# Optimization experiments

Measured on AMD Instinct MI355X. Metric: run time of the kernel, lower is better.

Reference implementation:

```python
import jax, jax.numpy as jnp
import numpy as np

D = 1024
H = 16
HD = D // H
FF = 2 * D
EPS = 1e-5


def _ln(x, g, b):
    mu = jnp.mean(x, axis=-1, keepdims=True)
    var = jnp.mean(jnp.square(x - mu), axis=-1, keepdims=True)
    return (x - mu) * jax.lax.rsqrt(var + EPS) * g + b


def setup_inputs() -> dict:
    key = jax.random.key(0)
    ks = jax.random.split(key, 16)
    s = 1.0 / np.sqrt(D)
    sf = 1.0 / np.sqrt(FF)
    inp = {
        "x": jax.random.normal(ks[0], (4, 2048, D), dtype=jnp.float32),
        "Wq": jax.random.uniform(ks[1], (D, D), jnp.float32, -s, s),
        "bq": jnp.zeros((D,), jnp.float32),
        "Wk": jax.random.uniform(ks[2], (D, D), jnp.float32, -s, s),
        "bk": jnp.zeros((D,), jnp.float32),
        "Wv": jax.random.uniform(ks[3], (D, D), jnp.float32, -s, s),
        "bv": jnp.zeros((D,), jnp.float32),
        "Wo": jax.random.uniform(ks[4], (D, D), jnp.float32, -s, s),
        "bo": jnp.zeros((D,), jnp.float32),
        "g1": jnp.ones((D,), jnp.float32),
        "b1": jnp.zeros((D,), jnp.float32),
        "g2": jnp.ones((D,), jnp.float32),
        "b2": jnp.zeros((D,), jnp.float32),
        "W1": jax.random.uniform(ks[5], (D, FF), jnp.float32, -s, s),
        "bf1": jnp.zeros((FF,), jnp.float32),
        "W2": jax.random.uniform(ks[6], (FF, D), jnp.float32, -sf, sf),
        "bf2": jnp.zeros((D,), jnp.float32),
    }
    return inp


def reference(x, Wq, bq, Wk, bk, Wv, bv, Wo, bo, g1, b1, g2, b2, W1, bf1, W2, bf2):
    B, S, _ = x.shape
    scale = HD ** -0.5
    residual = x
    xn = _ln(x, g1, b1)
    # QKV projections -> [B, H, S, HD]
    q = (xn @ Wq + bq).reshape(B, S, H, HD).transpose(0, 2, 1, 3)
    k = (xn @ Wk + bk).reshape(B, S, H, HD).transpose(0, 2, 1, 3)
    v = (xn @ Wv + bv).reshape(B, S, H, HD).transpose(0, 2, 1, 3)
    scores = jnp.einsum("bhqd,bhkd->bhqk", q, k) * scale
    attn = jax.nn.softmax(scores, axis=-1)  # dropout is identity at eval
    ctx = jnp.einsum("bhqk,bhkd->bhqd", attn, v)
    ctx = ctx.transpose(0, 2, 1, 3).reshape(B, S, D)
    x = ctx @ Wo + bo + residual
    residual = x
    xn = _ln(x, g2, b2)
    h = jax.nn.gelu(xn @ W1 + bf1, approximate=False)
    return h @ W2 + bf2 + residual
```

## Files before the change

### kernel.cpp

```cpp
#include <hip/hip_runtime.h>
#include <hip/hip_bf16.h>
#include <math.h>

#define D_MODEL 1024
#define H_NUM 16
#define HD 64
#define FF_DIM 2048
#define SEQ 2048
#define BATCH 4
#define M_TOK 8192

typedef __attribute__((ext_vector_type(8))) short bf16x8;
typedef __attribute__((ext_vector_type(4))) float f32x4;
typedef __attribute__((ext_vector_type(16))) float f32x16;
typedef __attribute__((ext_vector_type(4))) unsigned int uint4v;
typedef __attribute__((ext_vector_type(2))) int int2v;

__device__ __forceinline__ short f2bf(float f) {
  __hip_bfloat16 h = __float2bfloat16(f);
  return *reinterpret_cast<short*>(&h);
}

__device__ __forceinline__ void gload16(const void* g, void* l) {
  __builtin_amdgcn_global_load_lds((const __attribute__((address_space(1))) void*)g,
                                   (__attribute__((address_space(3))) void*)l, 16, 0, 0);
}

__device__ __forceinline__ unsigned cvt_pk_bf16(float lo, float hi) {
  unsigned r;
  asm("v_cvt_pk_bf16_f32 %0, %1, %2" : "=v"(r) : "v"(lo), "v"(hi));
  return r;
}

__device__ __forceinline__ float fexp2(float x) {
  float r;
  asm("v_exp_f32 %0, %1" : "=v"(r) : "v"(x));
  return r;
}

__device__ __forceinline__ float frcp(float x) {
  float r;
  asm("v_rcp_f32 %0, %1" : "=v"(r) : "v"(x));
  return r;
}

__device__ __forceinline__ float fmax3(float a, float b, float c) {
  float r;
  asm("v_max3_f32 %0, %1, %2, %3" : "=v"(r) : "v"(a), "v"(b), "v"(c));
  return r;
}

#define BARRIER() __builtin_amdgcn_s_barrier()
#define LGKM0()                                  \
  do {                                           \
    asm volatile("s_waitcnt lgkmcnt(0)");        \
    __builtin_amdgcn_sched_barrier(0);           \
  } while (0)
#define VMC(n)                                   \
  do {                                           \
    asm volatile("s_waitcnt vmcnt(" #n ")");     \
    __builtin_amdgcn_sched_barrier(0);           \
  } while (0)

__global__ __launch_bounds__(256) void transpose_all(
    const float* __restrict__ Wq, const float* __restrict__ Wk,
    const float* __restrict__ Wv, const float* __restrict__ Wo,
    const float* __restrict__ W1, const float* __restrict__ W2,
    short* __restrict__ WqkvT, short* __restrict__ WoT,
    short* __restrict__ W1T, short* __restrict__ W2T) {
  const int bid = blockIdx.x;
  const float* src;
  short* dst;
  int K, N, t;
  if (bid < 256)       { src = Wq; dst = WqkvT;           K = 1024; N = 1024; t = bid; }
  else if (bid < 512)  { src = Wk; dst = WqkvT + 1048576; K = 1024; N = 1024; t = bid - 256; }
  else if (bid < 768)  { src = Wv; dst = WqkvT + 2097152; K = 1024; N = 1024; t = bid - 512; }
  else if (bid < 1024) { src = Wo; dst = WoT;             K = 1024; N = 1024; t = bid - 768; }
  else if (bid < 1536) { src = W1; dst = W1T;             K = 1024; N = 2048; t = bid - 1024; }
  else                 { src = W2; dst = W2T;             K = 2048; N = 1024; t = bid - 1536; }
  const int lg = (N == 2048) ? 5 : 4;
  const int ty = t >> lg, tx = t & ((1 << lg) - 1);
  const int n0 = tx * 64, k0 = ty * 64;

  __shared__ float tile[64][65];
  const int tr = threadIdx.x >> 4;
  const int tc = (threadIdx.x & 15) * 4;
#pragma unroll
  for (int i = 0; i < 4; ++i) {
    int kr = tr + i * 16;
    float4 v = *(const float4*)(src + (size_t)(k0 + kr) * N + n0 + tc);
    tile[kr][tc] = v.x; tile[kr][tc + 1] = v.y; tile[kr][tc + 2] = v.z; tile[kr][tc + 3] = v.w;
  }
  __syncthreads();
#pragma unroll
  for (int i = 0; i < 4; ++i) {
    int r = tr + i * 16;
    short4 o;
    o.x = f2bf(tile[tc][r]);
    o.y = f2bf(tile[tc + 1][r]);
    o.z = f2bf(tile[tc + 2][r]);
    o.w = f2bf(tile[tc + 3][r]);
    *(short4*)(dst + (size_t)(n0 + r) * K + k0 + tc) = o;
  }
}

__global__ __launch_bounds__(256) void transpose_v(const short* __restrict__ src,
                                                   short* __restrict__ dst) {
  __shared__ short t[64][72];
  const int s0 = blockIdx.x * 64;
  const size_t b = (size_t)blockIdx.y * SEQ * HD;
  const int r = threadIdx.x >> 2;
  const int c = (threadIdx.x & 3) * 16;
  *(bf16x8*)&t[r][c] = *(const bf16x8*)(src + b + (size_t)(s0 + r) * HD + c);
  *(bf16x8*)&t[r][c + 8] = *(const bf16x8*)(src + b + (size_t)(s0 + r) * HD + c + 8);
  __syncthreads();
  const int d = threadIdx.x >> 2;
  const int cc = (threadIdx.x & 3) * 16;
  bf16x8 o0, o1;
#pragma unroll
  for (int i = 0; i < 8; ++i) o0[i] = t[cc + i][d];
#pragma unroll
  for (int i = 0; i < 8; ++i) o1[i] = t[cc + 8 + i][d];
  *(bf16x8*)(dst + b + (size_t)d * SEQ + s0 + cc) = o0;
  *(bf16x8*)(dst + b + (size_t)d * SEQ + s0 + cc + 8) = o1;
}

__global__ __launch_bounds__(256) void ln_bf16(const float* __restrict__ x,
                                               const float* __restrict__ g,
                                               const float* __restrict__ b,
                                               short* __restrict__ out) {
  const int row = blockIdx.x;
  const int t = threadIdx.x;
  const float* xr = x + (size_t)row * D_MODEL;
  float4 v = *(const float4*)(xr + t * 4);
  float s = v.x + v.y + v.z + v.w;
  float s2 = v.x * v.x + v.y * v.y + v.z * v.z + v.w * v.w;
#pragma unroll
  for (int m = 1; m < 64; m <<= 1) { s += __shfl_xor(s, m); s2 += __shfl_xor(s2, m); }
  __shared__ float ps[8];
  const int wid = t >> 6, lane = t & 63;
  if (lane == 0) { ps[wid] = s; ps[wid + 4] = s2; }
  __syncthreads();
  s = ps[0] + ps[1] + ps[2] + ps[3];
  s2 = ps[4] + ps[5] + ps[6] + ps[7];
  float mu = s * (1.f / D_MODEL);
  float rstd = rsqrtf(s2 * (1.f / D_MODEL) - mu * mu + 1e-5f);
  float4 gv = *(const float4*)(g + t * 4);
  float4 bv = *(const float4*)(b + t * 4);
  short4 o;
  o.x = f2bf((v.x - mu) * rstd * gv.x + bv.x);
  o.y = f2bf((v.y - mu) * rstd * gv.y + bv.y);
  o.z = f2bf((v.z - mu) * rstd * gv.z + bv.z);
  o.w = f2bf((v.w - mu) * rstd * gv.w + bv.w);
  *(short4*)(out + (size_t)row * D_MODEL + t * 4) = o;
}

template <int BM, int MODE>
__global__ __launch_bounds__(512, 2) void gemm_ring(const short* __restrict__ A,
                                                    const short* __restrict__ Bt,
                                                    const float* __restrict__ bias0,
                                                    const float* __restrict__ bias1,
                                                    const float* __restrict__ bias2,
                                                    const float* resid, float* outf,
                                                    short* outb0, short* outb1, short* outb2,
                                                    int M, int N, int K) {
  constexpr int FM = BM / 32;
  constexpr int GA = BM / 128;
  constexpr int ASLOT = BM * 32;
  constexpr int BSLOT = 256 * 32;
  constexpr int SLOT = ASLOT + BSLOT;
  __shared__ short lds[4 * SLOT];

  const int tid = threadIdx.x;
  const int lane = tid & 63;
  const int wid = tid >> 6;
  const int wr = wid >> 2, wc = wid & 3;
  const int l15 = lane & 15, l4 = lane >> 4;

  const int nwg = gridDim.x;
  const int id = blockIdx.x;
  const int swz = (id & 7) * (nwg >> 3) + (id >> 3);
  const int nbx = N >> 8;
  const int by = swz / nbx, bx = swz - by * nbx;
  const int row0 = by * BM, col0 = bx * 256;

  f32x4 acc[FM][4];
#pragma unroll
  for (int i = 0; i < FM; ++i)
#pragma unroll
    for (int j = 0; j < 4; ++j) acc[i][j] = (f32x4){0.f, 0.f, 0.f, 0.f};

  const int NH = K >> 5;

  auto STAGE = [&](int h) {
    const int k0 = h * 32;
    short* ab = lds + (h & 3) * SLOT;
#pragma unroll
    for (int s = 0; s < GA; ++s) {
      const int r = s * 128 + (tid >> 2);
      const int g = (tid & 3) ^ ((r >> 1) & 3);
      gload16(A + (size_t)(row0 + r) * K + k0 + g * 8, ab + s * 4096 + tid * 8);
    }
    short* bb = ab + ASLOT;
#pragma unroll
    for (int s = 0; s < 2; ++s) {
      const int r = s * 128 + (tid >> 2);
      const int g = (tid & 3) ^ ((r >> 1) & 3);
      gload16(Bt + (size_t)(col0 + r) * K + k0 + g * 8, bb + s * 4096 + tid * 8);
    }
  };

  bf16x8 Af[FM], Bf[4];

  STAGE(0);
  STAGE(1);
  STAGE(2);

  for (int h = 0; h < NH; ++h) {
    if (h + 2 < NH) {
      if constexpr (GA == 1) { VMC(6); } else { VMC(8); }
    } else if (h + 1 < NH) {
      if constexpr (GA == 1) { VMC(3); } else { VMC(4); }
    } else {
      VMC(0);
    }
    BARRIER();
    {
      const short* ab = lds + (h & 3) * SLOT;
#pragma unroll
      for (int i = 0; i < FM; ++i) {
        const int R = wr * (BM / 2) + i * 16 + l15;
        Af[i] = *(const bf16x8*)(ab + (R >> 1) * 64 + (R & 1) * 32 +
                                 ((l4 ^ ((R >> 1) & 3)) << 3));
      }
      const short* bb = ab + ASLOT;
#pragma unroll
      for (int nf = 0; nf < 4; ++nf) {
        const int R = wc * 64 + nf * 16 + l15;
        Bf[nf] = *(const bf16x8*)(bb + (R >> 1) * 64 + (R & 1) * 32 +
                                  ((l4 ^ ((R >> 1) & 3)) << 3));
      }
    }
    if (h + 3 < NH) STAGE(h + 3);
    LGKM0();
    __builtin_amdgcn_s_setprio(1);
#pragma unroll
    for (int i = 0; i < FM; ++i)
#pragma unroll
      for (int nf = 0; nf < 4; ++nf)
        acc[i][nf] = __builtin_amdgcn_mfma_f32_16x16x32_bf16(Af[i], Bf[nf], acc[i][nf], 0, 0, 0);
    __builtin_amdgcn_s_setprio(0);
  }

#pragma unroll
  for (int mf = 0; mf < FM; ++mf) {
#pragma unroll
    for (int nf = 0; nf < 4; ++nf) {
      const int rowb = row0 + wr * (BM / 2) + mf * 16 + (l4 << 2);
      const int col = col0 + wc * 64 + nf * 16 + l15;
      if (MODE == 0) {
        const int which = col >> 10, nn = col & 1023;
        const int hh = nn >> 6, dd = nn & 63;
        const float bias = (which == 0 ? bias0[nn] : which == 1 ? bias1[nn] : bias2[nn]);
        short* o = (which == 0 ? outb0 : which == 1 ? outb1 : outb2);
#pragma unroll
        for (int r = 0; r < 4; ++r) {
          const int row = rowb + r;
          float val = acc[mf][nf][r] + bias;
          if (which == 0) val *= 0.18033688011112042f;
          const int bb = row >> 11, s = row & 2047;
          const size_t dst = (((size_t)((bb << 4) + hh) << 11) + s) * HD + dd;
          o[dst] = f2bf(val);
        }
      } else {
#pragma unroll
        for (int r = 0; r < 4; ++r) {
          const int row = rowb + r;
          float val = acc[mf][nf][r];
          if (MODE == 2) {
            val += bias0[col];
            float a = val * val;
            float c1 = fmaf(a, 0.044715f, 1.0f);
            float arg = (val * 2.302116f) * c1;
            arg = fminf(fmaxf(arg, -60.f), 60.f);
            float e = fexp2(arg);
            float gl = val - val * frcp(e + 1.0f);
            outb0[(size_t)row * N + col] = f2bf(gl);
          } else {
            val += bias0[col] + resid[(size_t)row * N + col];
            outf[(size_t)row * N + col] = val;
          }
        }
      }
    }
  }
}

__global__ __launch_bounds__(256) void attn_swp(const short* __restrict__ q,
                                                const short* __restrict__ k,
                                                const short* __restrict__ vT,
                                                short* __restrict__ ctx) {
  __shared__ short Ks[2][4096];
  __shared__ short VTs[2][4096];
  const int tid = threadIdx.x;
  const int lane = tid & 63;
  const int wid = tid >> 6;
  const int hi = lane >> 5, l31 = lane & 31, l7 = lane & 7;
  const int qt = blockIdx.x, bh = blockIdx.y;
  const size_t base = (size_t)bh * SEQ * HD;
  const int q0 = qt * 128 + wid * 32;

  bf16x8 qf[4];
#pragma unroll
  for (int ks = 0; ks < 4; ++ks)
    qf[ks] = *(const bf16x8*)(q + base + (size_t)(q0 + l31) * HD + ks * 16 + hi * 8);

  bf16x8 onesv;
#pragma unroll
  for (int i = 0; i < 8; ++i) onesv[i] = (short)0x3F80;

  f32x16 o0, o1, o2;
#pragma unroll
  for (int r = 0; r < 16; ++r) { o0[r] = 0.f; o1[r] = 0.f; o2[r] = 0.f; }
  float mreg = -1e30f;

  const int sch = (tid & 7) ^ ((tid >> 3) & 7);

#define STAGE_AT(bi, kt)                                                            \
  {                                                                                 \
    const short* kb_ = k + base + (size_t)(kt) * 64 * HD;                           \
    const short* vb_ = vT + base + (size_t)(kt) * 64;                               \
    _Pragma("unroll") for (int p = 0; p < 2; ++p)                                   \
        gload16(kb_ + (size_t)(p * 32 + (tid >> 3)) * HD + sch * 8,                 \
                Ks[bi] + p * 2048 + tid * 8);                                       \
    _Pragma("unroll") for (int p = 0; p < 2; ++p)                                   \
        gload16(vb_ + (size_t)(p * 32 + (tid >> 3)) * SEQ + sch * 8,                \
                VTs[bi] + p * 2048 + tid * 8);                                      \
  }

  STAGE_AT(0, 0);
  __syncthreads();
  int cur = 0;

  for (int kt = 0; kt < SEQ / 64; ++kt) {
    if (kt + 1 < SEQ / 64) STAGE_AT(cur ^ 1, kt + 1);

    f32x16 s0, s1;
#pragma unroll
    for (int r = 0; r < 16; ++r) { s0[r] = 0.f; s1[r] = 0.f; }
#pragma unroll
    for (int ks = 0; ks < 4; ++ks) {
      const int ch = ((ks * 2 + hi) ^ l7) << 3;
      bf16x8 ka0 = *(const bf16x8*)(Ks[cur] + l31 * 64 + ch);
      bf16x8 ka1 = *(const bf16x8*)(Ks[cur] + (32 + l31) * 64 + ch);
      s0 = __builtin_amdgcn_mfma_f32_32x32x16_bf16(ka0, qf[ks], s0, 0, 0, 0);
      s1 = __builtin_amdgcn_mfma_f32_32x32x16_bf16(ka1, qf[ks], s1, 0, 0, 0);
    }

    float pm;
    {
      float t0 = fmax3(s0[0], s0[1], s0[2]);
      float t1 = fmax3(s0[3], s0[4], s0[5]);
      float t2 = fmax3(s0[6], s0[7], s0[8]);
      float t3 = fmax3(s0[9], s0[10], s0[11]);
      float t4 = fmax3(s0[12], s0[13], s0[14]);
      float t5 = fmax3(s0[15], s1[0], s1[1]);
      float t6 = fmax3(s1[2], s1[3], s1[4]);
      float t7 = fmax3(s1[5], s1[6], s1[7]);
      float t8 = fmax3(s1[8], s1[9], s1[10]);
      float t9 = fmax3(s1[11], s1[12], s1[13]);
      float ta = fmaxf(s1[14], s1[15]);
      float u0 = fmax3(t0, t1, t2);
      float u1 = fmax3(t3, t4, t5);
      float u2 = fmax3(t6, t7, t8);
      float u3 = fmaxf(t9, ta);
      pm = fmax3(fmaxf(u0, u1), u2, u3);
    }
    {
      int2v mm = __builtin_amdgcn_permlane32_swap(__builtin_bit_cast(int, pm),
                                                  __builtin_bit_cast(int, pm), false, false);
      pm = fmaxf(__builtin_bit_cast(float, mm[0]), __builtin_bit_cast(float, mm[1]));
    }
    if (!__all(pm <= mreg + 8.f)) {
      float mn = fmaxf(mreg, pm);
      float al = fexp2(mreg - mn);
      mreg = mn;
#pragma unroll
      for (int r = 0; r < 16; ++r) { o0[r] *= al; o1[r] *= al; o2[r] *= al; }
    }

#pragma unroll
    for (int r = 0; r < 16; ++r) s0[r] = fexp2(s0[r] - mreg);
#pragma unroll
    for (int r = 0; r < 16; ++r) s1[r] = fexp2(s1[r] - mreg);

    uint4v pw[4];
#pragma unroll
    for (int t = 0; t < 2; ++t) {
#pragma unroll
      for (int ks = 0; ks < 2; ++ks) {
        const f32x16& st = t ? s1 : s0;
        unsigned x0 = cvt_pk_bf16(st[8 * ks + 0], st[8 * ks + 1]);
        unsigned x1 = cvt_pk_bf16(st[8 * ks + 2], st[8 * ks + 3]);
        unsigned y0 = cvt_pk_bf16(st[8 * ks + 4], st[8 * ks + 5]);
        unsigned y1 = cvt_pk_bf16(st[8 * ks + 6], st[8 * ks + 7]);
        int2v a0 = __builtin_amdgcn_permlane32_swap((int)y0, (int)x0, false, false);
        int2v a1 = __builtin_amdgcn_permlane32_swap((int)y1, (int)x1, false, false);
        pw[t * 2 + ks] = (uint4v){(unsigned)a0[1], (unsigned)a1[1],
                                  (unsigned)a0[0], (unsigned)a1[0]};
      }
    }

#pragma unroll
    for (int s = 0; s < 4; ++s) {
      bf16x8 pf = __builtin_bit_cast(bf16x8, pw[s]);
      const int ch = ((s * 2 + hi) ^ l7) << 3;
      bf16x8 v0 = *(const bf16x8*)(VTs[cur] + l31 * 64 + ch);
      bf16x8 v1 = *(const bf16x8*)(VTs[cur] + (32 + l31) * 64 + ch);
      o0 = __builtin_amdgcn_mfma_f32_32x32x16_bf16(v0, pf, o0, 0, 0, 0);
      o1 = __builtin_amdgcn_mfma_f32_32x32x16_bf16(v1, pf, o1, 0, 0, 0);
      o2 = __builtin_amdgcn_mfma_f32_32x32x16_bf16(onesv, pf, o2, 0, 0, 0);
    }
    __syncthreads();
    cur ^= 1;
  }
#undef STAGE_AT

  const int b = bh >> 4, hh = bh & 15;
  const float inv = 1.f / o2[0];
  const size_t tokoff = ((size_t)(b * SEQ + q0 + l31)) * D_MODEL + hh * HD;
#pragma unroll
  for (int r = 0; r < 16; ++r) {
    const int d = (r & 3) + 8 * (r >> 2) + 4 * hi;
    ctx[tokoff + d] = f2bf(o0[r] * inv);
    ctx[tokoff + 32 + d] = f2bf(o1[r] * inv);
  }
}

extern "C" void kernel_launch(void* const* d_in, const int* in_sizes, int n_in,
                              void* d_out, int out_size, void* d_ws, size_t ws_size,
                              hipStream_t stream) {
  const float* x  = (const float*)d_in[0];
  const float* Wq = (const float*)d_in[1];
  const float* bq = (const float*)d_in[2];
  const float* Wk = (const float*)d_in[3];
  const float* bk = (const float*)d_in[4];
  const float* Wv = (const float*)d_in[5];
  const float* bv = (const float*)d_in[6];
  const float* Wo = (const float*)d_in[7];
  const float* bo = (const float*)d_in[8];
  const float* g1 = (const float*)d_in[9];
  const float* b1 = (const float*)d_in[10];
  const float* g2 = (const float*)d_in[11];
  const float* b2 = (const float*)d_in[12];
  const float* W1 = (const float*)d_in[13];
  const float* bf1 = (const float*)d_in[14];
  const float* W2 = (const float*)d_in[15];
  const float* bf2 = (const float*)d_in[16];

  char* w = (char*)d_ws;
  short* WqkvT = (short*)w; w += (size_t)3072 * 1024 * 2;
  short* WoT   = (short*)w; w += (size_t)1024 * 1024 * 2;
  short* W1T   = (short*)w; w += (size_t)2048 * 1024 * 2;
  short* W2T   = (short*)w; w += (size_t)1024 * 2048 * 2;
  short* xn    = (short*)w; w += (size_t)M_TOK * 1024 * 2;
  short* qb    = (short*)w; w += (size_t)M_TOK * 1024 * 2;
  short* kb    = (short*)w; w += (size_t)M_TOK * 1024 * 2;
  short* vTb   = (short*)w; w += (size_t)M_TOK * 1024 * 2;
  short* ctxb  = (short*)w; w += (size_t)M_TOK * 1024 * 2;
  short* xn2   = (short*)w; w += (size_t)M_TOK * 1024 * 2;
  short* hb    = (short*)w; w += (size_t)M_TOK * 2048 * 2;
  short* vb    = hb;

  dim3 blk(256);

  transpose_all<<<dim3(2048), blk, 0, stream>>>(Wq, Wk, Wv, Wo, W1, W2,
                                                WqkvT, WoT, W1T, W2T);

  ln_bf16<<<M_TOK, blk, 0, stream>>>(x, g1, b1, xn);

  gemm_ring<256, 0><<<dim3(12 * 32), dim3(512), 0, stream>>>(
      xn, WqkvT, bq, bk, bv, nullptr, nullptr, qb, kb, vb, M_TOK, 3072, 1024);

  transpose_v<<<dim3(SEQ / 64, BATCH * H_NUM), blk, 0, stream>>>(vb, vTb);

  attn_swp<<<dim3(16, 64), blk, 0, stream>>>(qb, kb, vTb, ctxb);

  gemm_ring<128, 1><<<dim3(4 * 64), dim3(512), 0, stream>>>(
      ctxb, WoT, bo, nullptr, nullptr, x, (float*)d_out, nullptr, nullptr, nullptr,
      M_TOK, 1024, 1024);

  ln_bf16<<<M_TOK, blk, 0, stream>>>((const float*)d_out, g2, b2, xn2);

  gemm_ring<256, 2><<<dim3(8 * 32), dim3(512), 0, stream>>>(
      xn2, W1T, bf1, nullptr, nullptr, nullptr, nullptr, hb, nullptr, nullptr,
      M_TOK, 2048, 1024);

  gemm_ring<128, 3><<<dim3(4 * 64), dim3(512), 0, stream>>>(
      hb, W2T, bf2, nullptr, nullptr, (const float*)d_out, (float*)d_out,
      nullptr, nullptr, nullptr, M_TOK, 1024, 2048);
}
```

Measured before the change: 317.1 us.

## Fuse LN1 into weight-prep kernel and use double-buffered 128-row QKV GEMM

Merges the first layernorm and the weight transpose/convert into one launch so both run concurrently. The QKV projection now uses a new gemm_ring2 kernel: 128-row tiles, double-buffered LDS and launch bounds that allow 4 workgroups per CU, giving more occupancy and a larger grid. The existing gemm_ring also moves its next-stage prefetch to right after the barrier, before the LDS fragment reads. This trades pipeline depth for occupancy and adds an extra barrier per iteration in gemm_ring2.

```diff
diff --git a/kernel.cpp b/kernel.cpp
--- a/kernel.cpp
+++ b/kernel.cpp
@@ -62,13 +62,43 @@
     __builtin_amdgcn_sched_barrier(0);           \
   } while (0)
 
-__global__ __launch_bounds__(256) void transpose_all(
+__global__ __launch_bounds__(256) void prep_fused(
+    const float* __restrict__ x, const float* __restrict__ g1,
+    const float* __restrict__ b1, short* __restrict__ xn,
     const float* __restrict__ Wq, const float* __restrict__ Wk,
     const float* __restrict__ Wv, const float* __restrict__ Wo,
     const float* __restrict__ W1, const float* __restrict__ W2,
     short* __restrict__ WqkvT, short* __restrict__ WoT,
     short* __restrict__ W1T, short* __restrict__ W2T) {
-  const int bid = blockIdx.x;
+  __shared__ float tile[64][65];
+  if (blockIdx.x < M_TOK) {
+    const int row = blockIdx.x;
+    const int t = threadIdx.x;
+    const float* xr = x + (size_t)row * D_MODEL;
+    float4 v = *(const float4*)(xr + t * 4);
+    float s = v.x + v.y + v.z + v.w;
+    float s2 = v.x * v.x + v.y * v.y + v.z * v.z + v.w * v.w;
+#pragma unroll
+    for (int m = 1; m < 64; m <<= 1) { s += __shfl_xor(s, m); s2 += __shfl_xor(s2, m); }
+    float* ps = &tile[0][0];
+    const int wid = t >> 6, lane = t & 63;
+    if (lane == 0) { ps[wid] = s; ps[wid + 4] = s2; }
+    __syncthreads();
+    s = ps[0] + ps[1] + ps[2] + ps[3];
+    s2 = ps[4] + ps[5] + ps[6] + ps[7];
+    float mu = s * (1.f / D_MODEL);
+    float rstd = rsqrtf(s2 * (1.f / D_MODEL) - mu * mu + 1e-5f);
+    float4 gv = *(const float4*)(g1 + t * 4);
+    float4 bv = *(const float4*)(b1 + t * 4);
+    short4 o;
+    o.x = f2bf((v.x - mu) * rstd * gv.x + bv.x);
+    o.y = f2bf((v.y - mu) * rstd * gv.y + bv.y);
+    o.z = f2bf((v.z - mu) * rstd * gv.z + bv.z);
+    o.w = f2bf((v.w - mu) * rstd * gv.w + bv.w);
+    *(short4*)(xn + (size_t)row * D_MODEL + t * 4) = o;
+    return;
+  }
+  const int bid = blockIdx.x - M_TOK;
   const float* src;
   short* dst;
   int K, N, t;
@@ -81,8 +111,6 @@
   const int lg = (N == 2048) ? 5 : 4;
   const int ty = t >> lg, tx = t & ((1 << lg) - 1);
   const int n0 = tx * 64, k0 = ty * 64;
-
-  __shared__ float tile[64][65];
   const int tr = threadIdx.x >> 4;
   const int tc = (threadIdx.x & 15) * 4;
 #pragma unroll
@@ -155,108 +183,18 @@
   *(short4*)(out + (size_t)row * D_MODEL + t * 4) = o;
 }
 
-template <int BM, int MODE>
-__global__ __launch_bounds__(512, 2) void gemm_ring(const short* __restrict__ A,
-                                                    const short* __restrict__ Bt,
-                                                    const float* __restrict__ bias0,
-                                                    const float* __restrict__ bias1,
-                                                    const float* __restrict__ bias2,
-                                                    const float* resid, float* outf,
-                                                    short* outb0, short* outb1, short* outb2,
-                                                    int M, int N, int K) {
-  constexpr int FM = BM / 32;
-  constexpr int GA = BM / 128;
-  constexpr int ASLOT = BM * 32;
-  constexpr int BSLOT = 256 * 32;
-  constexpr int SLOT = ASLOT + BSLOT;
-  __shared__ short lds[4 * SLOT];
-
-  const int tid = threadIdx.x;
-  const int lane = tid & 63;
-  const int wid = tid >> 6;
-  const int wr = wid >> 2, wc = wid & 3;
-  const int l15 = lane & 15, l4 = lane >> 4;
-
-  const int nwg = gridDim.x;
-  const int id = blockIdx.x;
-  const int swz = (id & 7) * (nwg >> 3) + (id >> 3);
-  const int nbx = N >> 8;
-  const int by = swz / nbx, bx = swz - by * nbx;
-  const int row0 = by * BM, col0 = bx * 256;
-
-  f32x4 acc[FM][4];
-#pragma unroll
-  for (int i = 0; i < FM; ++i)
-#pragma unroll
-    for (int j = 0; j < 4; ++j) acc[i][j] = (f32x4){0.f, 0.f, 0.f, 0.f};
-
-  const int NH = K >> 5;
-
-  auto STAGE = [&](int h) {
-    const int k0 = h * 32;
-    short* ab = lds + (h & 3) * SLOT;
-#pragma unroll
-    for (int s = 0; s < GA; ++s) {
-      const int r = s * 128 + (tid >> 2);
-      const int g = (tid & 3) ^ ((r >> 1) & 3);
-      gload16(A + (size_t)(row0 + r) * K + k0 + g * 8, ab + s * 4096 + tid * 8);
-    }
-    short* bb = ab + ASLOT;
-#pragma unroll
-    for (int s = 0; s < 2; ++s) {
-      const int r = s * 128 + (tid >> 2);
-      const int g = (tid & 3) ^ ((r >> 1) & 3);
-      gload16(Bt + (size_t)(col0 + r) * K + k0 + g * 8, bb + s * 4096 + tid * 8);
-    }
-  };
-
-  bf16x8 Af[FM], Bf[4];
-
-  STAGE(0);
-  STAGE(1);
-  STAGE(2);
-
-  for (int h = 0; h < NH; ++h) {
-    if (h + 2 < NH) {
-      if constexpr (GA == 1) { VMC(6); } else { VMC(8); }
-    } else if (h + 1 < NH) {
-      if constexpr (GA == 1) { VMC(3); } else { VMC(4); }
-    } else {
-      VMC(0);
-    }
-    BARRIER();
-    {
-      const short* ab = lds + (h & 3) * SLOT;
-#pragma unroll
-      for (int i = 0; i < FM; ++i) {
-        const int R = wr * (BM / 2) + i * 16 + l15;
-        Af[i] = *(const bf16x8*)(ab + (R >> 1) * 64 + (R & 1) * 32 +
-                                 ((l4 ^ ((R >> 1) & 3)) << 3));
-      }
-      const short* bb = ab + ASLOT;
-#pragma unroll
-      for (int nf = 0; nf < 4; ++nf) {
-        const int R = wc * 64 + nf * 16 + l15;
-        Bf[nf] = *(const bf16x8*)(bb + (R >> 1) * 64 + (R & 1) * 32 +
-                                  ((l4 ^ ((R >> 1) & 3)) << 3));
-      }
-    }
-    if (h + 3 < NH) STAGE(h + 3);
-    LGKM0();
-    __builtin_amdgcn_s_setprio(1);
-#pragma unroll
-    for (int i = 0; i < FM; ++i)
-#pragma unroll
-      for (int nf = 0; nf < 4; ++nf)
-        acc[i][nf] = __builtin_amdgcn_mfma_f32_16x16x32_bf16(Af[i], Bf[nf], acc[i][nf], 0, 0, 0);
-    __builtin_amdgcn_s_setprio(0);
-  }
-
+template <int FM, int MODE>
+__device__ __forceinline__ void gemm_epilogue(f32x4 (&acc)[FM][4], int row0, int col0,
+                                              int wr, int wc, int l15, int l4, int BMd2,
+                                              const float* bias0, const float* bias1,
+                                              const float* bias2, const float* resid,
+                                              float* outf, short* outb0, short* outb1,
+                                              short* outb2, int N) {
 #pragma unroll
   for (int mf = 0; mf < FM; ++mf) {
 #pragma unroll
     for (int nf = 0; nf < 4; ++nf) {
-      const int rowb = row0 + wr * (BM / 2) + mf * 16 + (l4 << 2);
+      const int rowb = row0 + wr * BMd2 + mf * 16 + (l4 << 2);
       const int col = col0 + wc * 64 + nf * 16 + l15;
       if (MODE == 0) {
         const int which = col >> 10, nn = col & 1023;
@@ -294,6 +232,201 @@
       }
     }
   }
+}
+
+template <int BM, int MODE>
+__global__ __launch_bounds__(512, 2) void gemm_ring(const short* __restrict__ A,
+                                                    const short* __restrict__ Bt,
+                                                    const float* __restrict__ bias0,
+                                                    const float* __restrict__ bias1,
+                                                    const float* __restrict__ bias2,
+                                                    const float* resid, float* outf,
+                                                    short* outb0, short* outb1, short* outb2,
+                                                    int M, int N, int K) {
+  constexpr int FM = BM / 32;
+  constexpr int GA = BM / 128;
+  constexpr int ASLOT = BM * 32;
+  constexpr int BSLOT = 256 * 32;
+  constexpr int SLOT = ASLOT + BSLOT;
+  __shared__ short lds[4 * SLOT];
+
+  const int tid = threadIdx.x;
+  const int lane = tid & 63;
+  const int wid = tid >> 6;
+  const int wr = wid >> 2, wc = wid & 3;
+  const int l15 = lane & 15, l4 = lane >> 4;
+
+  const int nwg = gridDim.x;
+  const int id = blockIdx.x;
+  const int swz = (id & 7) * (nwg >> 3) + (id >> 3);
+  const int nbx = N >> 8;
+  const int by = swz / nbx, bx = swz - by * nbx;
+  const int row0 = by * BM, col0 = bx * 256;
+
+  f32x4 acc[FM][4];
+#pragma unroll
+  for (int i = 0; i < FM; ++i)
+#pragma unroll
+    for (int j = 0; j < 4; ++j) acc[i][j] = (f32x4){0.f, 0.f, 0.f, 0.f};
+
+  const int NH = K >> 5;
+
+  auto STAGE = [&](int h) {
+    const int k0 = h * 32;
+    short* ab = lds + (h & 3) * SLOT;
+#pragma unroll
+    for (int s = 0; s < GA; ++s) {
+      const int r = s * 128 + (tid >> 2);
+      const int g = (tid & 3) ^ ((r >> 1) & 3);
+      gload16(A + (size_t)(row0 + r) * K + k0 + g * 8, ab + s * 4096 + tid * 8);
+    }
+    short* bb = ab + ASLOT;
+#pragma unroll
+    for (int s = 0; s < 2; ++s) {
+      const int r = s * 128 + (tid >> 2);
+      const int g = (tid & 3) ^ ((r >> 1) & 3);
+      gload16(Bt + (size_t)(col0 + r) * K + k0 + g * 8, bb + s * 4096 + tid * 8);
+    }
+  };
+
+  bf16x8 Af[FM], Bf[4];
+
+  STAGE(0);
+  STAGE(1);
+  STAGE(2);
+
+  for (int h = 0; h < NH; ++h) {
+    if (h + 2 < NH) {
+      if constexpr (GA == 1) { VMC(6); } else { VMC(8); }
+    } else if (h + 1 < NH) {
+      if constexpr (GA == 1) { VMC(3); } else { VMC(4); }
+    } else {
+      VMC(0);
+    }
+    BARRIER();
+    if (h + 3 < NH) STAGE(h + 3);
+    {
+      const short* ab = lds + (h & 3) * SLOT;
+#pragma unroll
+      for (int i = 0; i < FM; ++i) {
+        const int R = wr * (BM / 2) + i * 16 + l15;
+        Af[i] = *(const bf16x8*)(ab + (R >> 1) * 64 + (R & 1) * 32 +
+                                 ((l4 ^ ((R >> 1) & 3)) << 3));
+      }
+      const short* bb = ab + ASLOT;
+#pragma unroll
+      for (int nf = 0; nf < 4; ++nf) {
+        const int R = wc * 64 + nf * 16 + l15;
+        Bf[nf] = *(const bf16x8*)(bb + (R >> 1) * 64 + (R & 1) * 32 +
+                                  ((l4 ^ ((R >> 1) & 3)) << 3));
+      }
+    }
+    LGKM0();
+    __builtin_amdgcn_s_setprio(1);
+#pragma unroll
+    for (int i = 0; i < FM; ++i)
+#pragma unroll
+      for (int nf = 0; nf < 4; ++nf)
+        acc[i][nf] = __builtin_amdgcn_mfma_f32_16x16x32_bf16(Af[i], Bf[nf], acc[i][nf], 0, 0, 0);
+    __builtin_amdgcn_s_setprio(0);
+  }
+
+  gemm_epilogue<FM, MODE>(acc, row0, col0, wr, wc, l15, l4, BM / 2,
+                          bias0, bias1, bias2, resid, outf, outb0, outb1, outb2, N);
+}
+
+template <int MODE>
+__global__ __launch_bounds__(512, 4) void gemm_ring2(const short* __restrict__ A,
+                                                     const short* __restrict__ Bt,
+                                                     const float* __restrict__ bias0,
+                                                     const float* __restrict__ bias1,
+                                                     const float* __restrict__ bias2,
+                                                     const float* resid, float* outf,
+                                                     short* outb0, short* outb1, short* outb2,
+                                                     int M, int N, int K) {
+  constexpr int BM = 128;
+  constexpr int FM = 4;
+  constexpr int ASLOT = BM * 32;
+  constexpr int BSLOT = 256 * 32;
+  constexpr int SLOT = ASLOT + BSLOT;
+  __shared__ short lds[2 * SLOT];
+
+  const int tid = threadIdx.x;
+  const int lane = tid & 63;
+  const int wid = tid >> 6;
+  const int wr = wid >> 2, wc = wid & 3;
+  const int l15 = lane & 15, l4 = lane >> 4;
+
+  const int nwg = gridDim.x;
+  const int id = blockIdx.x;
+  const int swz = (id & 7) * (nwg >> 3) + (id >> 3);
+  const int nbx = N >> 8;
+  const int by = swz / nbx, bx = swz - by * nbx;
+  const int row0 = by * BM, col0 = bx * 256;
+
+  f32x4 acc[FM][4];
+#pragma unroll
+  for (int i = 0; i < FM; ++i)
+#pragma unroll
+    for (int j = 0; j < 4; ++j) acc[i][j] = (f32x4){0.f, 0.f, 0.f, 0.f};
+
+  const int NH = K >> 5;
+
+  auto STAGE = [&](int h) {
+    const int k0 = h * 32;
+    short* ab = lds + (h & 1) * SLOT;
+    {
+      const int r = tid >> 2;
+      const int g = (tid & 3) ^ ((r >> 1) & 3);
+      gload16(A + (size_t)(row0 + r) * K + k0 + g * 8, ab + tid * 8);
+    }
+    short* bb = ab + ASLOT;
+#pragma unroll
+    for (int s = 0; s < 2; ++s) {
+      const int r = s * 128 + (tid >> 2);
+      const int g = (tid & 3) ^ ((r >> 1) & 3);
+      gload16(Bt + (size_t)(col0 + r) * K + k0 + g * 8, bb + s * 4096 + tid * 8);
+    }
+  };
+
+  bf16x8 Af[FM], Bf[4];
+
+  STAGE(0);
+  STAGE(1);
+
+  for (int h = 0; h < NH; ++h) {
+    if (h + 1 < NH) { VMC(3); } else { VMC(0); }
+    BARRIER();
+    {
+      const short* ab = lds + (h & 1) * SLOT;
+#pragma unroll
+      for (int i = 0; i < FM; ++i) {
+        const int R = wr * (BM / 2) + i * 16 + l15;
+        Af[i] = *(const bf16x8*)(ab + (R >> 1) * 64 + (R & 1) * 32 +
+                                 ((l4 ^ ((R >> 1) & 3)) << 3));
+      }
+      const short* bb = ab + ASLOT;
+#pragma unroll
+      for (int nf = 0; nf < 4; ++nf) {
+        const int R = wc * 64 + nf * 16 + l15;
+        Bf[nf] = *(const bf16x8*)(bb + (R >> 1) * 64 + (R & 1) * 32 +
+                                  ((l4 ^ ((R >> 1) & 3)) << 3));
+      }
+    }
+    LGKM0();
+    BARRIER();
+    if (h + 2 < NH) STAGE(h + 2);
+    __builtin_amdgcn_s_setprio(1);
+#pragma unroll
+    for (int i = 0; i < FM; ++i)
+#pragma unroll
+      for (int nf = 0; nf < 4; ++nf)
+        acc[i][nf] = __builtin_amdgcn_mfma_f32_16x16x32_bf16(Af[i], Bf[nf], acc[i][nf], 0, 0, 0);
+    __builtin_amdgcn_s_setprio(0);
+  }
+
+  gemm_epilogue<FM, MODE>(acc, row0, col0, wr, wc, l15, l4, BM / 2,
+                          bias0, bias1, bias2, resid, outf, outb0, outb1, outb2, N);
 }
 
 __global__ __launch_bounds__(256) void attn_swp(const short* __restrict__ q,
@@ -474,12 +607,10 @@
 
   dim3 blk(256);
 
-  transpose_all<<<dim3(2048), blk, 0, stream>>>(Wq, Wk, Wv, Wo, W1, W2,
-                                                WqkvT, WoT, W1T, W2T);
-
-  ln_bf16<<<M_TOK, blk, 0, stream>>>(x, g1, b1, xn);
-
-  gemm_ring<256, 0><<<dim3(12 * 32), dim3(512), 0, stream>>>(
+  prep_fused<<<dim3(M_TOK + 2048), blk, 0, stream>>>(
+      x, g1, b1, xn, Wq, Wk, Wv, Wo, W1, W2, WqkvT, WoT, W1T, W2T);
+
+  gemm_ring2<0><<<dim3(12 * 64), dim3(512), 0, stream>>>(
       xn, WqkvT, bq, bk, bv, nullptr, nullptr, qb, kb, vb, M_TOK, 3072, 1024);
 
   transpose_v<<<dim3(SEQ / 64, BATCH * H_NUM), blk, 0, stream>>>(vb, vTb);
```

Result: no change. 314.5 us (-0.8%).
